# Kernel optimization log

Hardware: AMD Instinct MI355X
Metric: run time of the kernel (lower is better)

Reference implementation:

```python
import jax, jax.numpy as jnp
import numpy as np

B, S, D = 32, 200, 256          # batch, seq_len (hard-coded 200), emb_dim (hard-coded 256)
H_CLS, H_TNS, H = 2, 4, 6       # classical heads, tensor heads, total (rate=1/3, num_heads=6)
DFF, VOCAB, L, TD = 1024, 3500, 8, 2


def layer_norm(x, g, b, eps=1e-6):
    m = x.mean(-1, keepdims=True)
    v = ((x - m) ** 2).mean(-1, keepdims=True)
    return (x - m) * jax.lax.rsqrt(v + eps) * g + b


def setup_inputs() -> dict:
    key = jax.random.key(0)
    ks = jax.random.split(key, 12)
    n = jax.random.normal
    s1 = 1.0 / np.sqrt(4 + TD - 1.0)       # TNLayer RandomNormal stddev for A1/A4
    s2 = 1.0 / np.sqrt(4 + 2 * TD - 1.0)   # for A2/A3
    return {
        "tokens": jax.random.randint(ks[0], (B, S), 0, VOCAB),
        "tok_emb": n(ks[1], (VOCAB, D)) * 0.02,
        "pos_emb": n(ks[2], (S, D)) * 0.02,
        # stacked over L layers; axis 1 of size 3 is (q, k, v)
        "wqkv_w": n(ks[3], (L, 3, D, 2 * D)) * 0.05,
        "wqkv_b": jnp.zeros((L, 3, 2 * D)),
        "A1": n(ks[4], (L, 3, 4, TD, 4)) * s1,
        "A2": n(ks[5], (L, 3, 4, TD, TD, 8)) * s2,
        "A3": n(ks[6], (L, 3, 4, TD, TD, 8)) * s2,
        "A4": n(ks[7], (L, 3, 4, TD, 4)) * s1,
        "tnb": jnp.zeros((L, 3, 4 * D)),
        "out_w": n(ks[8], (L, H * D, D)) * 0.02,
        "out_b": jnp.zeros((L, D)),
        "ff1_w": n(ks[9], (L, D, DFF)) * 0.05,
        "ff1_b": jnp.zeros((L, DFF)),
        "ff2_w": n(ks[10], (L, DFF, D)) * 0.03,
        "ff2_b": jnp.zeros((L, D)),
        "ln1_g": jnp.ones((L, D)), "ln1_b": jnp.zeros((L, D)),
        "ln2_g": jnp.ones((L, D)), "ln2_b": jnp.zeros((L, D)),
    }


def bert_tensor_forward(tokens, tok_emb, pos_emb, wqkv_w, wqkv_b, A1, A2, A3, A4, tnb,
                        out_w, out_b, ff1_w, ff1_b, ff2_w, ff2_b, ln1_g, ln1_b, ln2_g, ln2_b):
    # embedding: positions array with start_index=1 is [0,1,...,199] -> pos_emb itself
    h = tok_emb[tokens] + pos_emb[None]                      # [B,S,D]
    # Attention_mask: 1.0 where token==0 (pad), broadcast over heads and query pos
    bias = (tokens == 0).astype(jnp.float32)[:, None, None, :] * (-1e9)  # [B,1,1,S]
    inv_sqrt_dk = 1.0 / jnp.sqrt(jnp.float32(D))

    def step(h, p):
        ww, wb, a1, a2, a3, a4, tb, ow, ob, f1w, f1b, f2w, f2b, g1, b1, g2, b2 = p
        # classical q/k/v heads: Dense(d_model * 2) -> [3,B,2,S,D]
        cls = jnp.einsum('bsd,xdf->xbsf', h, ww) + wb[:, None, None, :]
        cls = cls.reshape(3, B, S, H_CLS, D).transpose(0, 1, 3, 2, 4)
        # tensor-network q/k/v heads (TNLayer): MPO contraction over 4x4x4x4 split of D
        x6 = h.reshape(B, S, 4, 4, 4, 4)
        tns = jnp.einsum('bspqrt,xpmi,xqmnj,xrnok,xtol->xbsijkl', x6, a1, a2, a3, a4)
        tns = tns.reshape(3, B, S, 4 * D) + tb[:, None, None, :]
        tns = tns.reshape(3, B, S, H_TNS, D).transpose(0, 1, 3, 2, 4)  # [3,B,4,S,D]
        qkv = jnp.concatenate([cls, tns], axis=2)                      # [3,B,H,S,D]
        q, k, v = qkv[0], qkv[1], qkv[2]
        scores = jnp.einsum('bhqd,bhkd->bhqk', q, k) * inv_sqrt_dk + bias
        attn = jax.nn.softmax(scores, axis=-1)
        ctx = jnp.einsum('bhqk,bhkd->bhqd', attn, v)
        ctx = ctx.transpose(0, 2, 1, 3).reshape(B, S, H * D)           # [B,S,1536]
        out1 = layer_norm(h + ctx @ ow + ob, g1, b1)
        ffn = jax.nn.relu(out1 @ f1w + f1b) @ f2w + f2b
        return layer_norm(out1 + ffn, g2, b2), None

    xs = (wqkv_w, wqkv_b, A1, A2, A3, A4, tnb, out_w, out_b,
          ff1_w, ff1_b, ff2_w, ff2_b, ln1_g, ln1_b, ln2_g, ln2_b)
    h, _ = jax.lax.scan(step, h, xs)
    return h


def reference(tokens, tok_emb, pos_emb, wqkv_w, wqkv_b, A1, A2, A3, A4, tnb,
              out_w, out_b, ff1_w, ff1_b, ff2_w, ff2_b, ln1_g, ln1_b, ln2_g, ln2_b):
    return bert_tensor_forward(tokens, tok_emb, pos_emb, wqkv_w, wqkv_b, A1, A2, A3, A4,
                               tnb, out_w, out_b, ff1_w, ff1_b, ff2_w, ff2_b,
                               ln1_g, ln1_b, ln2_g, ln2_b)
```

## Files before the change

### kernel.cpp

```cpp
#include <hip/hip_runtime.h>
#include <hip/hip_bf16.h>

typedef __bf16 bf16x8 __attribute__((ext_vector_type(8)));
typedef float f32x4 __attribute__((ext_vector_type(4)));
typedef int i32x4 __attribute__((ext_vector_type(4)));

#define NB 32
#define NS 200
#define SP 256
#define ND 256
#define NH 6
#define NL 8
#define NBS (NB*NS)
#define NZ (NB*NH)
#define SLAB (SP*ND)
#define PSTR 264

using bf16 = __hip_bfloat16;

enum { EPI_F32 = 0, EPI_RELU_BF = 1 };

__device__ __forceinline__ float b2f(bf16 x) { return __bfloat162float(x); }
__device__ __forceinline__ bf16 f2b(float x) { return __float2bfloat16(x); }
__device__ __forceinline__ unsigned short fbits(float x) { bf16 h = f2b(x); return *(unsigned short*)&h; }

__device__ __forceinline__ void gload16(const bf16* g, const short* l) {
    __builtin_amdgcn_global_load_lds(
        (const __attribute__((address_space(1))) unsigned int*)(unsigned long long)(g),
        (__attribute__((address_space(3))) unsigned int*)(unsigned long long)(l), 16, 0, 0);
}

#define GUNIT(lane) ((((lane) & 3) ^ (((lane) >> 3) & 3)) * 8)
#define RUNIT(kcu, fr) ((((kcu) ^ (((fr) >> 1) & 3))) * 8)

__global__ __launch_bounds__(256)
void gemm_qkv(const bf16* __restrict__ A, const bf16* __restrict__ Bm,
              const float* __restrict__ qkvb, const float* __restrict__ tnbp,
              bf16* __restrict__ Qb, bf16* __restrict__ Kb, bf16* __restrict__ Vb)
{
    __shared__ __align__(16) char smem[32768];
    short* Asl0 = (short*)smem;
    short* Bsl0 = (short*)(smem + 16384);
    const int K = 256;
    const int tid  = threadIdx.x;
    const int m0   = blockIdx.y * 64;
    const int n0   = blockIdx.x * 64;
    const int lane = tid & 63, w = tid >> 6;
    const int wm   = (w >> 1) * 32, wn = (w & 1) * 32;
    const int fr   = lane & 15, kcu = lane >> 4;
    const int srow = lane >> 2, schk = GUNIT(lane);

    const bf16* Ag = A  + (long long)m0 * K;
    const bf16* Bg = Bm + (long long)n0 * K;

    f32x4 acc[2][2];
#pragma unroll
    for (int i = 0; i < 2; i++)
#pragma unroll
        for (int j = 0; j < 2; j++) acc[i][j] = (f32x4){0.f,0.f,0.f,0.f};

    auto stage = [&](int buf, int k0) {
        gload16(Ag + (long long)(w*16 + srow)*K + k0 + schk, &Asl0[buf*2048 + (w*16)*32]);
        gload16(Bg + (long long)(w*16 + srow)*K + k0 + schk, &Bsl0[buf*2048 + (w*16)*32]);
    };

    stage(0, 0);
    stage(1, 32);
    for (int t = 0; t < 8; t++) {
        const int buf = t & 3;
        if (t + 2 < 8) {
            stage((t + 2) & 3, (t + 2) * 32);
            asm volatile("s_waitcnt vmcnt(4)" ::: "memory");
        } else if (t + 1 < 8) {
            asm volatile("s_waitcnt vmcnt(2)" ::: "memory");
        } else {
            asm volatile("s_waitcnt vmcnt(0)" ::: "memory");
        }
        __builtin_amdgcn_s_barrier();
        __builtin_amdgcn_sched_barrier(0);
        bf16x8 af[2], bfm[2];
#pragma unroll
        for (int i = 0; i < 2; i++) af[i]  = *(const bf16x8*)&Asl0[buf*2048 + (wm + i*16 + fr)*32 + RUNIT(kcu, fr)];
#pragma unroll
        for (int j = 0; j < 2; j++) bfm[j] = *(const bf16x8*)&Bsl0[buf*2048 + (wn + j*16 + fr)*32 + RUNIT(kcu, fr)];
#pragma unroll
        for (int i = 0; i < 2; i++)
#pragma unroll
            for (int j = 0; j < 2; j++)
                acc[i][j] = __builtin_amdgcn_mfma_f32_16x16x32_bf16(af[i], bfm[j], acc[i][j], 0, 0, 0);
    }

    const int xq   = m0 / 1536;
    const int c1_0 = m0 - xq*1536;
    const int hdq  = c1_0 >> 8;
    const int ddb  = c1_0 & 255;

    if (xq < 2) {
        short* T = (short*)smem;
        __syncthreads();
#pragma unroll
        for (int i = 0; i < 2; i++) {
            const int dl0 = wm + i*16 + kcu*4;
            float bv[4];
#pragma unroll
            for (int rg = 0; rg < 4; rg++) {
                const int cc = c1_0 + dl0 + rg;
                bv[rg] = (cc < 512) ? qkvb[xq*512 + cc] : tnbp[xq*1024 + cc - 512];
            }
#pragma unroll
            for (int j = 0; j < 2; j++) {
                const int tok = wn + j*16 + fr;
                ushort4 pk;
                pk.x = fbits(acc[i][j][0] + bv[0]);
                pk.y = fbits(acc[i][j][1] + bv[1]);
                pk.z = fbits(acc[i][j][2] + bv[2]);
                pk.w = fbits(acc[i][j][3] + bv[3]);
                *(ushort4*)&T[tok*72 + dl0] = pk;
            }
        }
        __syncthreads();
        const int tt = tid >> 2;
        const int dc = (tid & 3) * 16;
        const int c  = n0 + tt;
        const int bb = c / NS, ss = c - bb*NS;
        bf16* dst = xq ? Kb : Qb;
        bf16* dp  = dst + ((long long)((bb*NH + hdq)*SP + ss))*ND + ddb + dc;
        *(i32x4*)dp       = *(const i32x4*)&T[tt*72 + dc];
        *(i32x4*)(dp + 8) = *(const i32x4*)&T[tt*72 + dc + 8];
    } else {
#pragma unroll
        for (int i = 0; i < 2; i++) {
            const int dl0 = wm + i*16 + kcu*4;
            float bv[4];
#pragma unroll
            for (int rg = 0; rg < 4; rg++) {
                const int cc = c1_0 + dl0 + rg;
                bv[rg] = (cc < 512) ? qkvb[2*512 + cc] : tnbp[2*1024 + cc - 512];
            }
#pragma unroll
            for (int j = 0; j < 2; j++) {
                const int c = n0 + wn + j*16 + fr;
                const int bb = c / NS, ss = c - bb*NS;
                const long long base = ((long long)((bb*NH + hdq)*ND + ddb + dl0))*SP + ss;
#pragma unroll
                for (int rg = 0; rg < 4; rg++)
                    Vb[base + (long long)rg*SP] = f2b(acc[i][j][rg] + bv[rg]);
            }
        }
    }
}

template<int MODE>
__global__ __launch_bounds__(256)
void gemm_nt(const bf16* __restrict__ A, const bf16* __restrict__ Bm,
             int M, int N, int K, int Kspan, long long sOz,
             float* __restrict__ outF, bf16* __restrict__ outBf,
             const float* __restrict__ bias)
{
    __shared__ short Asl[3][128*32];
    __shared__ short Bsl[3][128*32];
    const int tid  = threadIdx.x;
    const int m0   = blockIdx.y * 128;
    const int n0   = blockIdx.x * 128;
    const int kbase= blockIdx.z * Kspan;
    const int lane = tid & 63, w = tid >> 6;
    const int wm   = (w >> 1) * 64, wn = (w & 1) * 64;
    const int fr   = lane & 15, kc = (lane >> 4) * 8;
    const int srow = lane >> 2, schk = (lane & 3) * 8;

    const bf16* Ag = A  + (long long)m0 * K + kbase;
    const bf16* Bg = Bm + (long long)n0 * K + kbase;

    f32x4 acc[4][4];
#pragma unroll
    for (int i = 0; i < 4; i++)
#pragma unroll
        for (int j = 0; j < 4; j++) acc[i][j] = (f32x4){0.f,0.f,0.f,0.f};

    auto stage = [&](int buf, int k0) {
        gload16(Ag + (long long)(w*32      + srow)*K + k0 + schk, &Asl[buf][(w*32     )*32]);
        gload16(Ag + (long long)(w*32 + 16 + srow)*K + k0 + schk, &Asl[buf][(w*32 + 16)*32]);
        gload16(Bg + (long long)(w*32      + srow)*K + k0 + schk, &Bsl[buf][(w*32     )*32]);
        gload16(Bg + (long long)(w*32 + 16 + srow)*K + k0 + schk, &Bsl[buf][(w*32 + 16)*32]);
    };

    const int nt = Kspan >> 5;
    stage(0, 0);
    for (int t = 0; t < nt; t++) {
        const int buf = t % 3;
        if (t + 1 < nt) {
            stage((t + 1) % 3, (t + 1) * 32);
            asm volatile("s_waitcnt vmcnt(4)" ::: "memory");
        } else {
            asm volatile("s_waitcnt vmcnt(0)" ::: "memory");
        }
        __builtin_amdgcn_s_barrier();
        __builtin_amdgcn_sched_barrier(0);
        bf16x8 af[4], bfm[4];
#pragma unroll
        for (int i = 0; i < 4; i++) af[i]  = *(const bf16x8*)&Asl[buf][(wm + i*16 + fr)*32 + kc];
#pragma unroll
        for (int j = 0; j < 4; j++) bfm[j] = *(const bf16x8*)&Bsl[buf][(wn + j*16 + fr)*32 + kc];
#pragma unroll
        for (int i = 0; i < 4; i++)
#pragma unroll
            for (int j = 0; j < 4; j++)
                acc[i][j] = __builtin_amdgcn_mfma_f32_16x16x32_bf16(af[i], bfm[j], acc[i][j], 0, 0, 0);
    }

    const int rq = (lane >> 4) * 4;
#pragma unroll
    for (int i = 0; i < 4; i++) {
        const int r0 = m0 + wm + i*16 + rq;
#pragma unroll
        for (int j = 0; j < 4; j++) {
            const int c = n0 + wn + j*16 + fr;
            if (MODE == EPI_F32) {
#pragma unroll
                for (int rg = 0; rg < 4; rg++)
                    outF[(long long)blockIdx.z * sOz + (long long)(r0+rg)*N + c] = acc[i][j][rg];
            } else {
                const float bv = bias[c];
#pragma unroll
                for (int rg = 0; rg < 4; rg++)
                    outBf[(long long)(r0+rg)*N + c] = f2b(fmaxf(acc[i][j][rg] + bv, 0.f));
            }
        }
    }
}

__global__ __launch_bounds__(256)
void attn_fused(const bf16* __restrict__ Qb, const bf16* __restrict__ Kb,
                const bf16* __restrict__ Vtb, const int* __restrict__ tokens,
                bf16* __restrict__ ctx)
{
    __shared__ __align__(16) char smem[2*20480 + 1024 + 1024 + 64*PSTR*2];
    float* red   = (float*)(smem + 40960);
    float* maskv = (float*)(smem + 40960 + 1024);
    short* P     = (short*)(smem + 40960 + 2048);

    const int z  = blockIdx.x;
    const int b  = z / NH, h = z - b*NH;
    const int q0 = blockIdx.y * 64;
    const int tid = threadIdx.x;
    const int lane = tid & 63, w = tid >> 6;
    const int fr = lane & 15, qh = lane >> 4;
    const int kc = qh * 8;
    const int srow = lane >> 2, schk = GUNIT(lane);

    const bf16* Kp = Kb  + (long long)z * SLAB;
    const bf16* Qp = Qb  + (long long)z * SLAB;
    const bf16* Vp = Vtb + (long long)z * SLAB;

    {
        const int s = tid;
        float mv = -1e9f;
        if (s < NS && tokens[b*NS + s] != 0) mv = 0.f;
        maskv[s] = mv;
    }

    auto stage1 = [&](int buf, int k0) {
        short* Ks = (short*)(smem + buf*20480);
        short* Qs = (short*)(smem + buf*20480 + 16384);
#pragma unroll
        for (int r2 = 0; r2 < 4; r2++)
            gload16(Kp + (long long)(w*64 + r2*16 + srow)*ND + k0 + schk, &Ks[(w*64 + r2*16)*32]);
        gload16(Qp + (long long)(q0 + w*16 + srow)*ND + k0 + schk, &Qs[(w*16)*32]);
    };

    f32x4 acc[4][4];
#pragma unroll
    for (int i = 0; i < 4; i++)
#pragma unroll
        for (int j = 0; j < 4; j++) acc[i][j] = (f32x4){0.f,0.f,0.f,0.f};

    stage1(0, 0);
    for (int t = 0; t < 8; t++) {
        const int buf = t & 1;
        if (t + 1 < 8) {
            stage1(buf ^ 1, (t + 1) * 32);
            asm volatile("s_waitcnt vmcnt(5)" ::: "memory");
        } else {
            asm volatile("s_waitcnt vmcnt(0)" ::: "memory");
        }
        __builtin_amdgcn_s_barrier();
        __builtin_amdgcn_sched_barrier(0);
        const short* Ks = (const short*)(smem + buf*20480);
        const short* Qs = (const short*)(smem + buf*20480 + 16384);
        bf16x8 ak[4], bq[4];
#pragma unroll
        for (int i = 0; i < 4; i++) ak[i] = *(const bf16x8*)&Ks[(w*64 + i*16 + fr)*32 + RUNIT(qh, fr)];
#pragma unroll
        for (int j = 0; j < 4; j++) bq[j] = *(const bf16x8*)&Qs[(j*16 + fr)*32 + RUNIT(qh, fr)];
#pragma unroll
        for (int i = 0; i < 4; i++)
#pragma unroll
            for (int j = 0; j < 4; j++)
                acc[i][j] = __builtin_amdgcn_mfma_f32_16x16x32_bf16(ak[i], bq[j], acc[i][j], 0, 0, 0);
        __builtin_amdgcn_s_barrier();
        __builtin_amdgcn_sched_barrier(0);
    }

    float mk[4][4];
#pragma unroll
    for (int i = 0; i < 4; i++)
#pragma unroll
        for (int rg = 0; rg < 4; rg++) mk[i][rg] = maskv[w*64 + i*16 + qh*4 + rg];
#pragma unroll
    for (int i = 0; i < 4; i++)
#pragma unroll
        for (int j = 0; j < 4; j++)
#pragma unroll
            for (int rg = 0; rg < 4; rg++)
                acc[i][j][rg] = acc[i][j][rg] * 0.0625f + mk[i][rg];

    float pm[4];
#pragma unroll
    for (int j = 0; j < 4; j++) {
        float m = -3.0e38f;
#pragma unroll
        for (int i = 0; i < 4; i++)
#pragma unroll
            for (int rg = 0; rg < 4; rg++) m = fmaxf(m, acc[i][j][rg]);
        m = fmaxf(m, __shfl_xor(m, 16));
        m = fmaxf(m, __shfl_xor(m, 32));
        pm[j] = m;
    }
#pragma unroll
    for (int j = 0; j < 4; j++) red[w*64 + j*16 + fr] = pm[j];
    __syncthreads();
    float gm[4];
#pragma unroll
    for (int j = 0; j < 4; j++)
        gm[j] = fmaxf(fmaxf(red[j*16 + fr], red[64 + j*16 + fr]),
                      fmaxf(red[128 + j*16 + fr], red[192 + j*16 + fr]));
    float ps[4] = {0.f, 0.f, 0.f, 0.f};
#pragma unroll
    for (int i = 0; i < 4; i++)
#pragma unroll
        for (int j = 0; j < 4; j++)
#pragma unroll
            for (int rg = 0; rg < 4; rg++) {
                float e = __expf(acc[i][j][rg] - gm[j]);
                acc[i][j][rg] = e;
                ps[j] += e;
            }
#pragma unroll
    for (int j = 0; j < 4; j++) {
        ps[j] += __shfl_xor(ps[j], 16);
        ps[j] += __shfl_xor(ps[j], 32);
    }
    __syncthreads();
#pragma unroll
    for (int j = 0; j < 4; j++) red[w*64 + j*16 + fr] = ps[j];
    __syncthreads();
    float inv[4];
#pragma unroll
    for (int j = 0; j < 4; j++)
        inv[j] = 1.f / (red[j*16 + fr] + red[64 + j*16 + fr] + red[128 + j*16 + fr] + red[192 + j*16 + fr]);

#pragma unroll
    for (int i = 0; i < 4; i++)
#pragma unroll
        for (int j = 0; j < 4; j++) {
            ushort4 pk;
            pk.x = fbits(acc[i][j][0] * inv[j]);
            pk.y = fbits(acc[i][j][1] * inv[j]);
            pk.z = fbits(acc[i][j][2] * inv[j]);
            pk.w = fbits(acc[i][j][3] * inv[j]);
            *(ushort4*)&P[(j*16 + fr)*PSTR + w*64 + i*16 + qh*4] = pk;
        }
    __syncthreads();

    auto stage2 = [&](int buf, int s0) {
        short* Vs = (short*)(smem + buf*20480);
#pragma unroll
        for (int r2 = 0; r2 < 4; r2++)
            gload16(Vp + (long long)(w*64 + r2*16 + srow)*SP + s0 + schk, &Vs[(w*64 + r2*16)*32]);
    };

    f32x4 acc2[4][4];
#pragma unroll
    for (int i = 0; i < 4; i++)
#pragma unroll
        for (int j = 0; j < 4; j++) acc2[i][j] = (f32x4){0.f,0.f,0.f,0.f};

    stage2(0, 0);
    for (int t = 0; t < 7; t++) {
        const int buf = t & 1;
        if (t + 1 < 7) {
            stage2(buf ^ 1, (t + 1) * 32);
            asm volatile("s_waitcnt vmcnt(4)" ::: "memory");
        } else {
            asm volatile("s_waitcnt vmcnt(0)" ::: "memory");
        }
        __builtin_amdgcn_s_barrier();
        __builtin_amdgcn_sched_barrier(0);
        const short* Vs = (const short*)(smem + buf*20480);
        bf16x8 ap[4], bv[4];
#pragma unroll
        for (int i = 0; i < 4; i++) ap[i] = *(const bf16x8*)&P[(i*16 + fr)*PSTR + t*32 + kc];
#pragma unroll
        for (int j = 0; j < 4; j++) bv[j] = *(const bf16x8*)&Vs[(w*64 + j*16 + fr)*32 + RUNIT(qh, fr)];
#pragma unroll
        for (int i = 0; i < 4; i++)
#pragma unroll
            for (int j = 0; j < 4; j++)
                acc2[i][j] = __builtin_amdgcn_mfma_f32_16x16x32_bf16(ap[i], bv[j], acc2[i][j], 0, 0, 0);
        __builtin_amdgcn_s_barrier();
        __builtin_amdgcn_sched_barrier(0);
    }

#pragma unroll
    for (int i = 0; i < 4; i++)
#pragma unroll
        for (int j = 0; j < 4; j++)
#pragma unroll
            for (int rg = 0; rg < 4; rg++) {
                const int qg = q0 + i*16 + qh*4 + rg;
                if (qg < NS) {
                    const int d = w*64 + j*16 + fr;
                    ctx[((long long)(b*NS + qg))*1536 + h*256 + d] = f2b(acc2[i][j][rg]);
                }
            }
}

__global__ void embed_kernel(const int* __restrict__ tokens, const float* __restrict__ tok_emb,
                             const float* __restrict__ pos_emb, float* __restrict__ hf,
                             bf16* __restrict__ hbf)
{
    long long q = (long long)blockIdx.x * 256 + threadIdx.x;
    if (q >= (long long)NBS * 64) return;
    long long r = q >> 6;
    int j = (int)(q & 63) * 4;
    int tk = tokens[r];
    int s  = (int)(r % NS);
    float4 tv = *(const float4*)(tok_emb + (long long)tk * ND + j);
    float4 pv = *(const float4*)(pos_emb + s * ND + j);
    float4 v = make_float4(tv.x+pv.x, tv.y+pv.y, tv.z+pv.z, tv.w+pv.w);
    *(float4*)(hf + r*ND + j) = v;
    ushort4 pk;
    pk.x = fbits(v.x); pk.y = fbits(v.y); pk.z = fbits(v.z); pk.w = fbits(v.w);
    *(ushort4*)(hbf + r*ND + j) = pk;
}

__global__ __launch_bounds__(256)
void transpose_tile(const float* __restrict__ in, bf16* __restrict__ out,
                    int R, int C, long long inL, long long outL, int outStride)
{
    __shared__ float tl[32][33];
    const int l  = blockIdx.z;
    const int r0 = blockIdx.y * 32, c0 = blockIdx.x * 32;
    const float* ip = in + (long long)l * inL;
    bf16* op = out + (long long)l * outL;
    const int tx = threadIdx.x & 31, ty = threadIdx.x >> 5;
#pragma unroll
    for (int i = 0; i < 4; i++) {
        const int r = r0 + ty + i*8;
        tl[ty + i*8][tx] = ip[(long long)r * C + c0 + tx];
    }
    __syncthreads();
#pragma unroll
    for (int i = 0; i < 4; i++) {
        const int c = c0 + ty + i*8;
        op[(long long)c * outStride + r0 + tx] = f2b(tl[tx][ty + i*8]);
    }
}

__global__ __launch_bounds__(256)
void build_wtns(const float* __restrict__ A1, const float* __restrict__ A2,
                const float* __restrict__ A3, const float* __restrict__ A4,
                bf16* __restrict__ wcat)
{
    int lx = blockIdx.x;
    __shared__ float a1s[32], a2s[128], a3s[128], a4s[32];
    int t = threadIdx.x;
    if (t < 32)  { a1s[t] = A1[lx*32 + t]; a4s[t] = A4[lx*32 + t]; }
    if (t < 128) { a2s[t] = A2[lx*128 + t]; a3s[t] = A3[lx*128 + t]; }
    __syncthreads();
    int d = t;
    int p = d >> 6, q = (d >> 4) & 3, rr = (d >> 2) & 3, tt = d & 3;
    for (int i = 0; i < 4; i++) {
        float w1_0 = a1s[(p*2 + 0)*4 + i];
        float w1_1 = a1s[(p*2 + 1)*4 + i];
        for (int j = 0; j < 8; j++) {
            float c1_0 = w1_0 * a2s[((q*2+0)*2+0)*8 + j] + w1_1 * a2s[((q*2+1)*2+0)*8 + j];
            float c1_1 = w1_0 * a2s[((q*2+0)*2+1)*8 + j] + w1_1 * a2s[((q*2+1)*2+1)*8 + j];
            for (int kk = 0; kk < 8; kk++) {
                float c2_0 = c1_0 * a3s[((rr*2+0)*2+0)*8 + kk] + c1_1 * a3s[((rr*2+1)*2+0)*8 + kk];
                float c2_1 = c1_0 * a3s[((rr*2+0)*2+1)*8 + kk] + c1_1 * a3s[((rr*2+1)*2+1)*8 + kk];
                for (int ll = 0; ll < 4; ll++) {
                    float sv = c2_0 * a4s[(tt*2 + 0)*4 + ll] + c2_1 * a4s[(tt*2 + 1)*4 + ll];
                    int e = ((i*8 + j)*8 + kk)*4 + ll;
                    wcat[((long long)lx * 1536 + 512 + e) * 256 + d] = f2b(sv);
                }
            }
        }
    }
}

__global__ __launch_bounds__(256)
void ln_kernel(const float* __restrict__ raw0, const float* __restrict__ raw1,
               const float* __restrict__ bias, const float* __restrict__ resid,
               const float* __restrict__ g, const float* __restrict__ bb,
               float* __restrict__ outF, bf16* __restrict__ outBf)
{
    int w = threadIdx.x >> 6, lane = threadIdx.x & 63;
    long long r = (long long)blockIdx.x * 4 + w;
    long long base = r * ND + lane * 4;
    float4 x  = *(const float4*)(resid + base);
    float4 y0 = *(const float4*)(raw0 + base);
    float4 y1 = *(const float4*)(raw1 + base);
    float4 bs = *(const float4*)(bias + lane * 4);
    x.x += y0.x + y1.x + bs.x;
    x.y += y0.y + y1.y + bs.y;
    x.z += y0.z + y1.z + bs.z;
    x.w += y0.w + y1.w + bs.w;
    float s = x.x + x.y + x.z + x.w;
#pragma unroll
    for (int o = 32; o; o >>= 1) s += __shfl_xor(s, o);
    float mean = s * (1.f/256.f);
    float vs = (x.x-mean)*(x.x-mean) + (x.y-mean)*(x.y-mean)
             + (x.z-mean)*(x.z-mean) + (x.w-mean)*(x.w-mean);
#pragma unroll
    for (int o = 32; o; o >>= 1) vs += __shfl_xor(vs, o);
    float rs = rsqrtf(vs * (1.f/256.f) + 1e-6f);
    float4 gv = *(const float4*)(g  + lane * 4);
    float4 bv = *(const float4*)(bb + lane * 4);
    float4 o4;
    o4.x = (x.x - mean) * rs * gv.x + bv.x;
    o4.y = (x.y - mean) * rs * gv.y + bv.y;
    o4.z = (x.z - mean) * rs * gv.z + bv.z;
    o4.w = (x.w - mean) * rs * gv.w + bv.w;
    *(float4*)(outF + base) = o4;
    ushort4 pk;
    pk.x = fbits(o4.x); pk.y = fbits(o4.y); pk.z = fbits(o4.z); pk.w = fbits(o4.w);
    *(ushort4*)(outBf + base) = pk;
}

extern "C" void kernel_launch(void* const* d_in, const int* in_sizes, int n_in,
                              void* d_out, int out_size, void* d_ws, size_t ws_size,
                              hipStream_t stream)
{
    const int*   tokens  = (const int*)  d_in[0];
    const float* tok_emb = (const float*)d_in[1];
    const float* pos_emb = (const float*)d_in[2];
    const float* wqkv_w  = (const float*)d_in[3];
    const float* wqkv_b  = (const float*)d_in[4];
    const float* A1      = (const float*)d_in[5];
    const float* A2      = (const float*)d_in[6];
    const float* A3      = (const float*)d_in[7];
    const float* A4      = (const float*)d_in[8];
    const float* tnb     = (const float*)d_in[9];
    const float* out_w   = (const float*)d_in[10];
    const float* out_b   = (const float*)d_in[11];
    const float* ff1_w   = (const float*)d_in[12];
    const float* ff1_b   = (const float*)d_in[13];
    const float* ff2_w   = (const float*)d_in[14];
    const float* ff2_b   = (const float*)d_in[15];
    const float* ln1_g   = (const float*)d_in[16];
    const float* ln1_b   = (const float*)d_in[17];
    const float* ln2_g   = (const float*)d_in[18];
    const float* ln2_b   = (const float*)d_in[19];

    char* ws = (char*)d_ws;
    size_t off = 0;
    auto alloc = [&](size_t bytes) -> char* {
        char* p = ws + off;
        off += (bytes + 255) & ~(size_t)255;
        return p;
    };
    float* hf    = (float*)alloc((size_t)NBS * ND * 4);
    bf16*  hbf   = (bf16*) alloc((size_t)NBS * ND * 2);
    bf16*  wcat  = (bf16*) alloc(24ull * 1536 * 256 * 2);
    bf16*  owt   = (bf16*) alloc(8ull * 256 * 1536 * 2);
    bf16*  f1wt  = (bf16*) alloc(8ull * 1024 * 256 * 2);
    bf16*  f2wt  = (bf16*) alloc(8ull * 256 * 1024 * 2);
    bf16*  Qb    = (bf16*) alloc((size_t)NZ * SLAB * 2);
    bf16*  Kb    = (bf16*) alloc((size_t)NZ * SLAB * 2);
    bf16*  Vtb   = (bf16*) alloc((size_t)NZ * SLAB * 2);
    bf16*  ctxg  = (bf16*) alloc((size_t)NBS * 1536 * 2);
    bf16*  ffn   = (bf16*) alloc((size_t)NBS * 1024 * 2);
    float* raw   = (float*)alloc((size_t)NBS * ND * 4 * 2);
    float* out1f = (float*)alloc((size_t)NBS * ND * 4);
    bf16*  out1bf= (bf16*) alloc((size_t)NBS * ND * 2);
    if (off > ws_size) return;
    float* raw1 = raw + (size_t)NBS * ND;


    embed_kernel<<<1600, 256, 0, stream>>>(tokens, tok_emb, pos_emb, hf, hbf);
    transpose_tile<<<dim3(16, 8, 24), 256, 0, stream>>>(
        wqkv_w, wcat, 256, 512, 256ll*512, 1536ll*256, 256);
    build_wtns<<<24, 256, 0, stream>>>(A1, A2, A3, A4, wcat);
    transpose_tile<<<dim3(8, 48, 8), 256, 0, stream>>>(
        out_w, owt, 1536, 256, 1536ll*256, 256ll*1536, 1536);
    transpose_tile<<<dim3(32, 8, 8), 256, 0, stream>>>(
        ff1_w, f1wt, 256, 1024, 256ll*1024, 1024ll*256, 256);
    transpose_tile<<<dim3(8, 32, 8), 256, 0, stream>>>(
        ff2_w, f2wt, 1024, 256, 1024ll*256, 256ll*1024, 1024);

    for (int l = 0; l < NL; l++) {
        const bf16* wl = wcat + (long long)l * 3 * 1536 * 256;
        gemm_qkv<<<dim3(100, 72, 1), 256, 0, stream>>>(
            wl, hbf, wqkv_b + l * 3 * 512, tnb + l * 3 * 1024, Qb, Kb, Vtb);
        attn_fused<<<dim3(NZ, 4), 256, 0, stream>>>(Qb, Kb, Vtb, tokens, ctxg);
        gemm_nt<EPI_F32><<<dim3(2, 50, 2), 256, 0, stream>>>(
            ctxg, owt + (long long)l * 256 * 1536, NBS, 256, 1536, 768, (long long)NBS*ND,
            raw, nullptr, nullptr);
        ln_kernel<<<1600, 256, 0, stream>>>(raw, raw1, out_b + l * 256, hf,
                                            ln1_g + l * 256, ln1_b + l * 256, out1f, out1bf);
        gemm_nt<EPI_RELU_BF><<<dim3(8, 50, 1), 256, 0, stream>>>(
            out1bf, f1wt + (long long)l * 1024 * 256, NBS, 1024, 256, 256, 0,
            nullptr, ffn, ff1_b + l * 1024);
        gemm_nt<EPI_F32><<<dim3(2, 50, 2), 256, 0, stream>>>(
            ffn, f2wt + (long long)l * 256 * 1024, NBS, 256, 1024, 512, (long long)NBS*ND,
            raw, nullptr, nullptr);
        ln_kernel<<<1600, 256, 0, stream>>>(raw, raw1, ff2_b + l * 256, out1f,
                                            ln2_g + l * 256, ln2_b + l * 256,
                                            (l == NL - 1) ? (float*)d_out : hf, hbf);
    }
}
```

Baseline: 947.9 us.

## Keep QKV weight tile in registers and sweep four token tiles per block

The QKV projection kernel now loads its 64x256 weight slab into LDS once, moves it into registers, and then loops over four consecutive 64-token tiles of activations. Each token tile is streamed through a 4-deep LDS ring, with the epilogue run once per tile. This removes the weight reload each block used to do, cutting A-operand traffic fourfold, and reduces the grid from 7200 to 1800 blocks. The cost is more register pressure (16 bf16x8 fragments held per thread), serialized epilogues inside each block, and fewer blocks available to hide latency.

```diff
diff --git a/kernel.cpp b/kernel.cpp
--- a/kernel.cpp
+++ b/kernel.cpp
@@ -24,6 +24,8 @@
 __device__ __forceinline__ bf16 f2b(float x) { return __float2bfloat16(x); }
 __device__ __forceinline__ unsigned short fbits(float x) { bf16 h = f2b(x); return *(unsigned short*)&h; }
 
+#define MFMA __builtin_amdgcn_mfma_f32_16x16x32_bf16
+
 __device__ __forceinline__ void gload16(const bf16* g, const short* l) {
     __builtin_amdgcn_global_load_lds(
         (const __attribute__((address_space(1))) unsigned int*)(unsigned long long)(g),
@@ -39,114 +41,136 @@
               bf16* __restrict__ Qb, bf16* __restrict__ Kb, bf16* __restrict__ Vb)
 {
     __shared__ __align__(16) char smem[32768];
-    short* Asl0 = (short*)smem;
-    short* Bsl0 = (short*)(smem + 16384);
+    short* Asl = (short*)smem;
+    short* Bsl = (short*)smem;
+    short* T   = (short*)(smem + 16384);
     const int K = 256;
     const int tid  = threadIdx.x;
     const int m0   = blockIdx.y * 64;
-    const int n0   = blockIdx.x * 64;
+    const int n0   = blockIdx.x * 256;
     const int lane = tid & 63, w = tid >> 6;
     const int wm   = (w >> 1) * 32, wn = (w & 1) * 32;
     const int fr   = lane & 15, kcu = lane >> 4;
     const int srow = lane >> 2, schk = GUNIT(lane);
 
-    const bf16* Ag = A  + (long long)m0 * K;
-    const bf16* Bg = Bm + (long long)n0 * K;
-
-    f32x4 acc[2][2];
-#pragma unroll
-    for (int i = 0; i < 2; i++)
-#pragma unroll
-        for (int j = 0; j < 2; j++) acc[i][j] = (f32x4){0.f,0.f,0.f,0.f};
-
-    auto stage = [&](int buf, int k0) {
-        gload16(Ag + (long long)(w*16 + srow)*K + k0 + schk, &Asl0[buf*2048 + (w*16)*32]);
-        gload16(Bg + (long long)(w*16 + srow)*K + k0 + schk, &Bsl0[buf*2048 + (w*16)*32]);
-    };
-
-    stage(0, 0);
-    stage(1, 32);
-    for (int t = 0; t < 8; t++) {
-        const int buf = t & 3;
-        if (t + 2 < 8) {
-            stage((t + 2) & 3, (t + 2) * 32);
-            asm volatile("s_waitcnt vmcnt(4)" ::: "memory");
-        } else if (t + 1 < 8) {
-            asm volatile("s_waitcnt vmcnt(2)" ::: "memory");
-        } else {
-            asm volatile("s_waitcnt vmcnt(0)" ::: "memory");
-        }
-        __builtin_amdgcn_s_barrier();
-        __builtin_amdgcn_sched_barrier(0);
-        bf16x8 af[2], bfm[2];
-#pragma unroll
-        for (int i = 0; i < 2; i++) af[i]  = *(const bf16x8*)&Asl0[buf*2048 + (wm + i*16 + fr)*32 + RUNIT(kcu, fr)];
-#pragma unroll
-        for (int j = 0; j < 2; j++) bfm[j] = *(const bf16x8*)&Bsl0[buf*2048 + (wn + j*16 + fr)*32 + RUNIT(kcu, fr)];
+    const bf16* Ag = A + (long long)m0 * K;
+
+#pragma unroll
+    for (int c = 0; c < 8; c++)
+        gload16(Ag + (long long)(w*16 + srow)*K + c*32 + schk, &Asl[c*2048 + (w*16)*32]);
+    asm volatile("s_waitcnt vmcnt(0)" ::: "memory");
+    __builtin_amdgcn_s_barrier();
+    __builtin_amdgcn_sched_barrier(0);
+    bf16x8 afr[2][8];
+#pragma unroll
+    for (int c = 0; c < 8; c++)
 #pragma unroll
         for (int i = 0; i < 2; i++)
-#pragma unroll
-            for (int j = 0; j < 2; j++)
-                acc[i][j] = __builtin_amdgcn_mfma_f32_16x16x32_bf16(af[i], bfm[j], acc[i][j], 0, 0, 0);
-    }
+            afr[i][c] = *(const bf16x8*)&Asl[c*2048 + (wm + i*16 + fr)*32 + RUNIT(kcu, fr)];
+    asm volatile("s_waitcnt lgkmcnt(0)" ::: "memory");
+    __builtin_amdgcn_sched_barrier(0);
+    __builtin_amdgcn_s_barrier();
+    __builtin_amdgcn_sched_barrier(0);
 
     const int xq   = m0 / 1536;
     const int c1_0 = m0 - xq*1536;
     const int hdq  = c1_0 >> 8;
     const int ddb  = c1_0 & 255;
 
-    if (xq < 2) {
-        short* T = (short*)smem;
-        __syncthreads();
-#pragma unroll
-        for (int i = 0; i < 2; i++) {
-            const int dl0 = wm + i*16 + kcu*4;
-            float bv[4];
-#pragma unroll
-            for (int rg = 0; rg < 4; rg++) {
-                const int cc = c1_0 + dl0 + rg;
-                bv[rg] = (cc < 512) ? qkvb[xq*512 + cc] : tnbp[xq*1024 + cc - 512];
+    auto stageB = [&](int g) {
+        const int nt4 = g >> 3, ts = g & 7, buf = g & 3;
+        gload16(Bm + (long long)(n0 + nt4*64 + w*16 + srow)*K + ts*32 + schk,
+                &Bsl[buf*2048 + (w*16)*32]);
+    };
+
+    f32x4 acc[2][2];
+#pragma unroll
+    for (int i = 0; i < 2; i++)
+#pragma unroll
+        for (int j = 0; j < 2; j++) acc[i][j] = (f32x4){0.f,0.f,0.f,0.f};
+
+    stageB(0);
+    stageB(1);
+    for (int nt4 = 0; nt4 < 4; nt4++) {
+#pragma unroll
+        for (int t = 0; t < 8; t++) {
+            const int g = nt4*8 + t;
+            const int buf = g & 3;
+            if (g + 2 < 32) {
+                stageB(g + 2);
+                asm volatile("s_waitcnt vmcnt(2)" ::: "memory");
+            } else if (g + 1 < 32) {
+                asm volatile("s_waitcnt vmcnt(1)" ::: "memory");
+            } else {
+                asm volatile("s_waitcnt vmcnt(0)" ::: "memory");
             }
-#pragma unroll
-            for (int j = 0; j < 2; j++) {
-                const int tok = wn + j*16 + fr;
-                ushort4 pk;
-                pk.x = fbits(acc[i][j][0] + bv[0]);
-                pk.y = fbits(acc[i][j][1] + bv[1]);
-                pk.z = fbits(acc[i][j][2] + bv[2]);
-                pk.w = fbits(acc[i][j][3] + bv[3]);
-                *(ushort4*)&T[tok*72 + dl0] = pk;
+            __builtin_amdgcn_s_barrier();
+            __builtin_amdgcn_sched_barrier(0);
+            bf16x8 b0 = *(const bf16x8*)&Bsl[buf*2048 + (wn      + fr)*32 + RUNIT(kcu, fr)];
+            bf16x8 b1 = *(const bf16x8*)&Bsl[buf*2048 + (wn + 16 + fr)*32 + RUNIT(kcu, fr)];
+            acc[0][0] = MFMA(afr[0][t], b0, acc[0][0], 0, 0, 0);
+            acc[0][1] = MFMA(afr[0][t], b1, acc[0][1], 0, 0, 0);
+            acc[1][0] = MFMA(afr[1][t], b0, acc[1][0], 0, 0, 0);
+            acc[1][1] = MFMA(afr[1][t], b1, acc[1][1], 0, 0, 0);
+        }
+
+        const int nb = n0 + nt4*64;
+        if (xq < 2) {
+            __syncthreads();
+#pragma unroll
+            for (int i = 0; i < 2; i++) {
+                const int dl0 = wm + i*16 + kcu*4;
+                float bv[4];
+#pragma unroll
+                for (int rg = 0; rg < 4; rg++) {
+                    const int cc = c1_0 + dl0 + rg;
+                    bv[rg] = (cc < 512) ? qkvb[xq*512 + cc] : tnbp[xq*1024 + cc - 512];
+                }
+#pragma unroll
+                for (int j = 0; j < 2; j++) {
+                    const int tok = wn + j*16 + fr;
+                    ushort4 pk;
+                    pk.x = fbits(acc[i][j][0] + bv[0]);
+                    pk.y = fbits(acc[i][j][1] + bv[1]);
+                    pk.z = fbits(acc[i][j][2] + bv[2]);
+                    pk.w = fbits(acc[i][j][3] + bv[3]);
+                    *(ushort4*)&T[tok*72 + dl0] = pk;
+                }
             }
-        }
-        __syncthreads();
-        const int tt = tid >> 2;
-        const int dc = (tid & 3) * 16;
-        const int c  = n0 + tt;
-        const int bb = c / NS, ss = c - bb*NS;
-        bf16* dst = xq ? Kb : Qb;
-        bf16* dp  = dst + ((long long)((bb*NH + hdq)*SP + ss))*ND + ddb + dc;
-        *(i32x4*)dp       = *(const i32x4*)&T[tt*72 + dc];
-        *(i32x4*)(dp + 8) = *(const i32x4*)&T[tt*72 + dc + 8];
-    } else {
-#pragma unroll
-        for (int i = 0; i < 2; i++) {
-            const int dl0 = wm + i*16 + kcu*4;
-            float bv[4];
-#pragma unroll
-            for (int rg = 0; rg < 4; rg++) {
-                const int cc = c1_0 + dl0 + rg;
-                bv[rg] = (cc < 512) ? qkvb[2*512 + cc] : tnbp[2*1024 + cc - 512];
+            __syncthreads();
+            const int tt = tid >> 2;
+            const int dc = (tid & 3) * 16;
+            const int c  = nb + tt;
+            const int bb = c / NS, ss = c - bb*NS;
+            bf16* dst = xq ? Kb : Qb;
+            bf16* dp  = dst + ((long long)((bb*NH + hdq)*SP + ss))*ND + ddb + dc;
+            *(i32x4*)dp       = *(const i32x4*)&T[tt*72 + dc];
+            *(i32x4*)(dp + 8) = *(const i32x4*)&T[tt*72 + dc + 8];
+        } else {
+#pragma unroll
+            for (int i = 0; i < 2; i++) {
+                const int dl0 = wm + i*16 + kcu*4;
+                float bv[4];
+#pragma unroll
+                for (int rg = 0; rg < 4; rg++) {
+                    const int cc = c1_0 + dl0 + rg;
+                    bv[rg] = (cc < 512) ? qkvb[2*512 + cc] : tnbp[2*1024 + cc - 512];
+                }
+#pragma unroll
+                for (int j = 0; j < 2; j++) {
+                    const int c = nb + wn + j*16 + fr;
+                    const int bb = c / NS, ss = c - bb*NS;
+                    const long long base = ((long long)((bb*NH + hdq)*ND + ddb + dl0))*SP + ss;
+#pragma unroll
+                    for (int rg = 0; rg < 4; rg++)
+                        Vb[base + (long long)rg*SP] = f2b(acc[i][j][rg] + bv[rg]);
+                }
             }
-#pragma unroll
-            for (int j = 0; j < 2; j++) {
-                const int c = n0 + wn + j*16 + fr;
-                const int bb = c / NS, ss = c - bb*NS;
-                const long long base = ((long long)((bb*NH + hdq)*ND + ddb + dl0))*SP + ss;
-#pragma unroll
-                for (int rg = 0; rg < 4; rg++)
-                    Vb[base + (long long)rg*SP] = f2b(acc[i][j][rg] + bv[rg]);
-            }
-        }
+        }
+#pragma unroll
+        for (int i = 0; i < 2; i++)
+#pragma unroll
+            for (int j = 0; j < 2; j++) acc[i][j] = (f32x4){0.f,0.f,0.f,0.f};
     }
 }
 
@@ -205,7 +229,7 @@
         for (int i = 0; i < 4; i++)
 #pragma unroll
             for (int j = 0; j < 4; j++)
-                acc[i][j] = __builtin_amdgcn_mfma_f32_16x16x32_bf16(af[i], bfm[j], acc[i][j], 0, 0, 0);
+                acc[i][j] = MFMA(af[i], bfm[j], acc[i][j], 0, 0, 0);
     }
 
     const int rq = (lane >> 4) * 4;
@@ -296,7 +320,7 @@
         for (int i = 0; i < 4; i++)
 #pragma unroll
             for (int j = 0; j < 4; j++)
-                acc[i][j] = __builtin_amdgcn_mfma_f32_16x16x32_bf16(ak[i], bq[j], acc[i][j], 0, 0, 0);
+                acc[i][j] = MFMA(ak[i], bq[j], acc[i][j], 0, 0, 0);
         __builtin_amdgcn_s_barrier();
         __builtin_amdgcn_sched_barrier(0);
     }
@@ -406,7 +430,7 @@
         for (int i = 0; i < 4; i++)
 #pragma unroll
             for (int j = 0; j < 4; j++)
-                acc2[i][j] = __builtin_amdgcn_mfma_f32_16x16x32_bf16(ap[i], bv[j], acc2[i][j], 0, 0, 0);
+                acc2[i][j] = MFMA(ap[i], bv[j], acc2[i][j], 0, 0, 0);
         __builtin_amdgcn_s_barrier();
         __builtin_amdgcn_sched_barrier(0);
     }
@@ -601,7 +625,7 @@
 
     for (int l = 0; l < NL; l++) {
         const bf16* wl = wcat + (long long)l * 3 * 1536 * 256;
-        gemm_qkv<<<dim3(100, 72, 1), 256, 0, stream>>>(
+        gemm_qkv<<<dim3(25, 72, 1), 256, 0, stream>>>(
             wl, hbf, wqkv_b + l * 3 * 512, tnb + l * 3 * 1024, Qb, Kb, Vtb);
         attn_fused<<<dim3(NZ, 4), 256, 0, stream>>>(Qb, Kb, Vtb, tokens, ctxg);
         gemm_nt<EPI_F32><<<dim3(2, 50, 2), 256, 0, stream>>>(
```

Measured after the change: 986.8 us. +4.1%, slower.
